# Optimization experiments

Measured on AMD Instinct MI355X. Metric: run time of the kernel, lower is better.

## Reference

```python
import jax, jax.numpy as jnp
import numpy as np

T, B = 21, 4096
H, E, V = 1024, 50, 96
PAD = 0


def setup_inputs() -> dict:
    key = jax.random.key(0)
    ks = jax.random.split(key, 10)
    s_e = 1.0 / np.sqrt(H)  # torch LSTM init scale
    emb = jax.random.normal(ks[0], (V, E), jnp.float32)
    emb = emb.at[PAD].set(0.0)  # padding_idx row is zero
    return {
        "input_ids": jax.random.randint(ks[1], (T, B), 0, V),
        "h0": jax.random.normal(ks[2], (1, B, H), jnp.float32),
        "c0": jax.random.normal(ks[3], (1, B, H), jnp.float32),
        "emb": emb,
        "W_ih": jax.random.uniform(ks[4], (4 * H, E), jnp.float32, -s_e, s_e),
        "W_hh": jax.random.uniform(ks[5], (4 * H, H), jnp.float32, -s_e, s_e),
        "b_ih": jax.random.uniform(ks[6], (4 * H,), jnp.float32, -s_e, s_e),
        "b_hh": jax.random.uniform(ks[7], (4 * H,), jnp.float32, -s_e, s_e),
        "W_out": jax.random.uniform(ks[8], (V, H), jnp.float32, -s_e, s_e),
        "b_out": jax.random.uniform(ks[9], (V,), jnp.float32, -s_e, s_e),
    }


def reference(input_ids, h0, c0, emb, W_ih, W_hh, b_ih, b_hh, W_out, b_out):
    # char_embeds: (T, B, E)
    x = emb[input_ids]
    # Precompute input projections for all timesteps in one GEMM: (T, B, 4H)
    x_proj = jnp.einsum("tbe,ge->tbg", x, W_ih) + b_ih + b_hh

    def step(carry, xp_t):
        h, c = carry  # (B, H) each
        gates = xp_t + h @ W_hh.T  # (B, 4H), torch gate order i,f,g,o
        i, f, g, o = jnp.split(gates, 4, axis=-1)
        i = jax.nn.sigmoid(i)
        f = jax.nn.sigmoid(f)
        g = jnp.tanh(g)
        o = jax.nn.sigmoid(o)
        c = f * c + i * g
        h = o * jnp.tanh(c)
        return (h, c), h

    (h_T, c_T), h_ts = jax.lax.scan(step, (h0[0], c0[0]), x_proj)
    # char_output_projection: (T, B, V)
    scores = jnp.einsum("tbh,vh->tbv", h_ts, W_out) + b_out
    return scores, (h_T[None], c_T[None])
```

## Files before the change

### kernel.cpp

```cpp
#include <hip/hip_runtime.h>
#include <hip/hip_bf16.h>


#define T_STEPS 21
#define BSZ 4096
#define HDIM 1024
#define VOCAB 96
#define EDIM 50

typedef __attribute__((ext_vector_type(8))) short short8;
typedef __attribute__((ext_vector_type(4))) float f32x4;

#define GLL16(g, l)                                                        \
  __builtin_amdgcn_global_load_lds(                                        \
      (const __attribute__((address_space(1))) void*)(g),                  \
      (__attribute__((address_space(3))) void*)(l), 16, 0, 0)

__device__ __forceinline__ float sigmoidf_fast(float x) {
  return 1.0f / (1.0f + __expf(-x));
}
__device__ __forceinline__ float tanhf_fast(float x) {
  return 2.0f / (1.0f + __expf(-2.0f * x)) - 1.0f;
}

__global__ void prep_convert(const float* __restrict__ Whh_f,
                             const float* __restrict__ Wout_f,
                             const float* __restrict__ h0,
                             __hip_bfloat16* __restrict__ Whh,
                             __hip_bfloat16* __restrict__ Wout,
                             __hip_bfloat16* __restrict__ hb0) {
  int idx = blockIdx.x * 256 + threadIdx.x;
  if (idx < 4 * HDIM * HDIM) {
    Whh[idx] = __float2bfloat16(Whh_f[idx]);
    hb0[idx] = __float2bfloat16(h0[idx]);
  }
  if (idx < VOCAB * HDIM) Wout[idx] = __float2bfloat16(Wout_f[idx]);
}

__global__ void prep_ptable(const float* __restrict__ emb,
                            const float* __restrict__ Wih,
                            const float* __restrict__ bih,
                            const float* __restrict__ bhh,
                            __hip_bfloat16* __restrict__ Pb) {
  int idx = blockIdx.x * 256 + threadIdx.x;
  int v = idx >> 12, g = idx & 4095;
  int gate = g >> 10, j = g & 1023;
  const float* er = emb + v * EDIM;
  const float* wr = Wih + g * EDIM;
  float s = bih[g] + bhh[g];
#pragma unroll 10
  for (int e = 0; e < EDIM; ++e) s += er[e] * wr[e];
  Pb[(size_t)(j >> 5) * 12288 + v * 128 + gate * 32 + (j & 31)] =
      __float2bfloat16(s);
}

template <bool LAST>
__global__ __launch_bounds__(256, 3) void lstm_step_kernel(
    const int* __restrict__ ids,
    const __hip_bfloat16* __restrict__ hprev,
    const __hip_bfloat16* __restrict__ Whh,
    const __hip_bfloat16* __restrict__ Pb,
    const float* __restrict__ c_in,
    float* __restrict__ c_out,
    __hip_bfloat16* __restrict__ hnext,
    float* __restrict__ hf32)
{
  __shared__ __align__(16) char smem[32768];
  __hip_bfloat16* sA = (__hip_bfloat16*)smem;
  __hip_bfloat16* sB = (__hip_bfloat16*)(smem + 16384);
  __hip_bfloat16* sPb = (__hip_bfloat16*)smem;

  const int tid = threadIdx.x;
  const int wave = tid >> 6;
  const int lane = tid & 63;
  const int bid = blockIdx.x;
  const int jt = (bid & 7) * 4 + ((bid >> 3) & 3);
  const int mt = bid >> 5;
  const int m0 = mt * 128;
  const int j0 = jt * 32;

  f32x4 acc[4][4] = {};

  const int lrow = lane >> 3;
  const int lcol = ((lane & 7) ^ lrow) * 8;

  int brow_g[4];
#pragma unroll
  for (int i = 0; i < 4; ++i) {
    int n = wave * 32 + i * 8 + lrow;
    int q = n >> 6, gate = (n >> 4) & 3, u = n & 15;
    brow_g[i] = gate * HDIM + j0 + q * 16 + u;
  }
  const __hip_bfloat16* Abase =
      hprev + (size_t)(m0 + wave * 32 + lrow) * HDIM + lcol;

  const int mw = (wave >> 1) * 64;
  const int gn = wave & 1;
  const int u16 = lane & 15;
  const int k16q = lane >> 4;

  const int jo = gn * 16 + u16;
  const int j = j0 + jo;
  const int rb = m0 + mw + k16q * 4;
  float cpre[4][4];
#pragma unroll
  for (int mi = 0; mi < 4; ++mi)
#pragma unroll
    for (int r = 0; r < 4; ++r)
      cpre[mi][r] = c_in[(size_t)(rb + mi * 16 + r) * HDIM + j];

  for (int k0 = 0; k0 < HDIM; k0 += 64) {
#pragma unroll
    for (int i = 0; i < 4; ++i) {
      GLL16(Abase + i * 8 * HDIM + k0, &sA[(wave * 32 + i * 8) * 64]);
      GLL16(Whh + (size_t)brow_g[i] * HDIM + k0 + lcol,
            &sB[(wave * 32 + i * 8) * 64]);
    }
    __syncthreads();
#pragma unroll
    for (int kk = 0; kk < 64; kk += 32) {
      const int sl = (((kk >> 3) + k16q) ^ (u16 & 7)) * 8;
      short8 af[4], bf[4];
#pragma unroll
      for (int mi = 0; mi < 4; ++mi)
        af[mi] = *(const short8*)&sA[(mw + mi * 16 + u16) * 64 + sl];
#pragma unroll
      for (int ni = 0; ni < 4; ++ni)
        bf[ni] = *(const short8*)&sB[(gn * 64 + ni * 16 + u16) * 64 + sl];
#pragma unroll
      for (int mi = 0; mi < 4; ++mi)
#pragma unroll
        for (int ni = 0; ni < 4; ++ni)
          acc[mi][ni] = __builtin_amdgcn_mfma_f32_16x16x32_bf16(
              af[mi], bf[ni], acc[mi][ni], 0, 0, 0);
    }
    __syncthreads();
  }

  {
    const __hip_bfloat16* Pbj = Pb + (size_t)jt * 12288;
#pragma unroll
    for (int i = 0; i < 6; ++i)
      GLL16(Pbj + (wave * 6 + i) * 512 + lane * 8, &sPb[(wave * 6 + i) * 512]);
  }
  __syncthreads();

#pragma unroll
  for (int mi = 0; mi < 4; ++mi) {
#pragma unroll
    for (int r = 0; r < 4; ++r) {
      int row = rb + mi * 16 + r;
      int id = ids[row];
      const __hip_bfloat16* Pr = &sPb[id * 128 + jo];
      float iv = acc[mi][0][r] + __bfloat162float(Pr[0]);
      float fv = acc[mi][1][r] + __bfloat162float(Pr[32]);
      float gv = acc[mi][2][r] + __bfloat162float(Pr[64]);
      float ov = acc[mi][3][r] + __bfloat162float(Pr[96]);
      iv = sigmoidf_fast(iv);
      fv = sigmoidf_fast(fv);
      gv = tanhf_fast(gv);
      ov = sigmoidf_fast(ov);
      size_t off = (size_t)row * HDIM + j;
      float cc = fv * cpre[mi][r] + iv * gv;
      c_out[off] = cc;
      float hh = ov * tanhf_fast(cc);
      hnext[off] = __float2bfloat16(hh);
      if (LAST) hf32[off] = hh;
    }
  }
}

__global__ __launch_bounds__(256, 2) void scores_kernel(
    const __hip_bfloat16* __restrict__ h,
    const __hip_bfloat16* __restrict__ Wout,
    const float* __restrict__ bout,
    float* __restrict__ out)
{
  __shared__ __align__(16) __hip_bfloat16 sA[128 * 128];
  __shared__ __align__(16) __hip_bfloat16 sB[96 * 128];

  const int tid = threadIdx.x;
  const int wave = tid >> 6, lane = tid & 63;
  const int u16 = lane & 15, k16q = lane >> 4;
  const long r0 = (long)blockIdx.x * 128;

  f32x4 acc[2][6] = {};

  const int srow4 = lane >> 4;
  const int sslot = lane & 15;

  for (int k0 = 0; k0 < HDIM; k0 += 128) {
#pragma unroll
    for (int i = 0; i < 8; ++i) {
      int row = wave * 32 + i * 4 + srow4;
      int gg = sslot ^ (row & 15);
      GLL16(h + (r0 + row) * HDIM + k0 + gg * 8, &sA[(wave * 32 + i * 4) * 128]);
    }
#pragma unroll
    for (int i = 0; i < 6; ++i) {
      int row = wave * 24 + i * 4 + srow4;
      int gg = sslot ^ (row & 15);
      GLL16(Wout + (size_t)row * HDIM + k0 + gg * 8,
            &sB[(wave * 24 + i * 4) * 128]);
    }
    __syncthreads();
#pragma unroll
    for (int kk = 0; kk < 128; kk += 32) {
      const int sl = (((kk >> 3) + k16q) ^ u16) * 8;
      short8 af[2], bf[6];
#pragma unroll
      for (int mi = 0; mi < 2; ++mi)
        af[mi] = *(const short8*)&sA[(wave * 32 + mi * 16 + u16) * 128 + sl];
#pragma unroll
      for (int ni = 0; ni < 6; ++ni)
        bf[ni] = *(const short8*)&sB[(ni * 16 + u16) * 128 + sl];
#pragma unroll
      for (int mi = 0; mi < 2; ++mi)
#pragma unroll
        for (int ni = 0; ni < 6; ++ni)
          acc[mi][ni] = __builtin_amdgcn_mfma_f32_16x16x32_bf16(
              af[mi], bf[ni], acc[mi][ni], 0, 0, 0);
    }
    __syncthreads();
  }

#pragma unroll
  for (int ni = 0; ni < 6; ++ni) {
    int v = ni * 16 + u16;
    float bv = bout[v];
#pragma unroll
    for (int mi = 0; mi < 2; ++mi)
#pragma unroll
      for (int r = 0; r < 4; ++r) {
        long grow = r0 + wave * 32 + mi * 16 + k16q * 4 + r;
        out[grow * VOCAB + v] = acc[mi][ni][r] + bv;
      }
  }
}

extern "C" void kernel_launch(void* const* d_in, const int* in_sizes, int n_in,
                              void* d_out, int out_size, void* d_ws, size_t ws_size,
                              hipStream_t stream) {
  const int* ids = (const int*)d_in[0];
  const float* h0 = (const float*)d_in[1];
  const float* c0 = (const float*)d_in[2];
  const float* emb = (const float*)d_in[3];
  const float* Wih = (const float*)d_in[4];
  const float* Whh_f = (const float*)d_in[5];
  const float* bih = (const float*)d_in[6];
  const float* bhh = (const float*)d_in[7];
  const float* Wout_f = (const float*)d_in[8];
  const float* bout = (const float*)d_in[9];

  float* out = (float*)d_out;
  float* scores = out;
  float* hT = out + (size_t)T_STEPS * BSZ * VOCAB;
  float* cT = hT + (size_t)BSZ * HDIM;

  const size_t BH = (size_t)BSZ * HDIM;
  char* w = (char*)d_ws;
  __hip_bfloat16* Pb = (__hip_bfloat16*)w;   w += (size_t)32 * 12288 * 2;
  __hip_bfloat16* Whh = (__hip_bfloat16*)w;  w += (size_t)4 * HDIM * HDIM * 2;
  __hip_bfloat16* Wout = (__hip_bfloat16*)w; w += (size_t)VOCAB * HDIM * 2;
  __hip_bfloat16* hts = (__hip_bfloat16*)w;
  size_t base = (size_t)32 * 12288 * 2 + (size_t)4 * HDIM * HDIM * 2 +
                (size_t)VOCAB * HDIM * 2;
  const bool full = ws_size >= base + (size_t)(T_STEPS + 1) * BH * 2;

  prep_convert<<<dim3((4 * HDIM * HDIM + 255) / 256), dim3(256), 0, stream>>>(
      Whh_f, Wout_f, h0, Whh, Wout, hts);
  prep_ptable<<<dim3((VOCAB * 4096) / 256), dim3(256), 0, stream>>>(
      emb, Wih, bih, bhh, Pb);

  for (int t = 0; t < T_STEPS; ++t) {
    __hip_bfloat16* hp = hts + (full ? (size_t)t * BH : (size_t)(t & 1) * BH);
    __hip_bfloat16* hn =
        hts + (full ? (size_t)(t + 1) * BH : (size_t)((t + 1) & 1) * BH);
    const float* cin = (t == 0) ? c0 : cT;
    if (t == T_STEPS - 1) {
      lstm_step_kernel<true><<<dim3(1024), dim3(256), 0, stream>>>(
          ids + (size_t)t * BSZ, hp, Whh, Pb, cin, cT, hn, hT);
    } else {
      lstm_step_kernel<false><<<dim3(1024), dim3(256), 0, stream>>>(
          ids + (size_t)t * BSZ, hp, Whh, Pb, cin, cT, hn, nullptr);
    }
    if (!full) {
      scores_kernel<<<dim3(BSZ / 128), dim3(256), 0, stream>>>(
          hn, Wout, bout, scores + (size_t)t * BSZ * VOCAB);
    }
  }
  if (full) {
    scores_kernel<<<dim3(T_STEPS * BSZ / 128), dim3(256), 0, stream>>>(
        hts + BH, Wout, bout, scores);
  }
}
```

Before: 1.188 ms.

## Double LSTM step M-tile to 256 rows for W_hh reuse

Each LSTM step block now computes 256 batch rows instead of 128, so every W_hh tile loaded into LDS feeds twice as many MFMAs and the grid halves to 512 blocks. Accumulators, cell-state prefetch and LDS grow to match, and launch bounds drop to 2 blocks per CU. This trades lower weight-load traffic for more register and LDS pressure and fewer blocks to hide latency with (512 blocks against 256 CUs).

```diff
diff --git a/kernel.cpp b/kernel.cpp
--- a/kernel.cpp
+++ b/kernel.cpp
@@ -55,7 +55,7 @@
 }
 
 template <bool LAST>
-__global__ __launch_bounds__(256, 3) void lstm_step_kernel(
+__global__ __launch_bounds__(256, 2) void lstm_step_kernel(
     const int* __restrict__ ids,
     const __hip_bfloat16* __restrict__ hprev,
     const __hip_bfloat16* __restrict__ Whh,
@@ -65,9 +65,9 @@
     __hip_bfloat16* __restrict__ hnext,
     float* __restrict__ hf32)
 {
-  __shared__ __align__(16) char smem[32768];
+  __shared__ __align__(16) char smem[49152];
   __hip_bfloat16* sA = (__hip_bfloat16*)smem;
-  __hip_bfloat16* sB = (__hip_bfloat16*)(smem + 16384);
+  __hip_bfloat16* sB = (__hip_bfloat16*)(smem + 32768);
   __hip_bfloat16* sPb = (__hip_bfloat16*)smem;
 
   const int tid = threadIdx.x;
@@ -76,10 +76,10 @@
   const int bid = blockIdx.x;
   const int jt = (bid & 7) * 4 + ((bid >> 3) & 3);
   const int mt = bid >> 5;
-  const int m0 = mt * 128;
+  const int m0 = mt * 256;
   const int j0 = jt * 32;
 
-  f32x4 acc[4][4] = {};
+  f32x4 acc[2][4][4] = {};
 
   const int lrow = lane >> 3;
   const int lcol = ((lane & 7) ^ lrow) * 8;
@@ -92,7 +92,7 @@
     brow_g[i] = gate * HDIM + j0 + q * 16 + u;
   }
   const __hip_bfloat16* Abase =
-      hprev + (size_t)(m0 + wave * 32 + lrow) * HDIM + lcol;
+      hprev + (size_t)(m0 + wave * 64 + lrow) * HDIM + lcol;
 
   const int mw = (wave >> 1) * 64;
   const int gn = wave & 1;
@@ -101,38 +101,48 @@
 
   const int jo = gn * 16 + u16;
   const int j = j0 + jo;
-  const int rb = m0 + mw + k16q * 4;
-  float cpre[4][4];
-#pragma unroll
-  for (int mi = 0; mi < 4; ++mi)
-#pragma unroll
-    for (int r = 0; r < 4; ++r)
-      cpre[mi][r] = c_in[(size_t)(rb + mi * 16 + r) * HDIM + j];
+  int rb[2];
+  rb[0] = m0 + mw + k16q * 4;
+  rb[1] = m0 + 128 + mw + k16q * 4;
+  float cpre[2][4][4];
+#pragma unroll
+  for (int t = 0; t < 2; ++t)
+#pragma unroll
+    for (int mi = 0; mi < 4; ++mi)
+#pragma unroll
+      for (int r = 0; r < 4; ++r)
+        cpre[t][mi][r] = c_in[(size_t)(rb[t] + mi * 16 + r) * HDIM + j];
 
   for (int k0 = 0; k0 < HDIM; k0 += 64) {
 #pragma unroll
-    for (int i = 0; i < 4; ++i) {
-      GLL16(Abase + i * 8 * HDIM + k0, &sA[(wave * 32 + i * 8) * 64]);
+    for (int i = 0; i < 8; ++i)
+      GLL16(Abase + i * 8 * HDIM + k0, &sA[(wave * 64 + i * 8) * 64]);
+#pragma unroll
+    for (int i = 0; i < 4; ++i)
       GLL16(Whh + (size_t)brow_g[i] * HDIM + k0 + lcol,
             &sB[(wave * 32 + i * 8) * 64]);
-    }
     __syncthreads();
 #pragma unroll
     for (int kk = 0; kk < 64; kk += 32) {
       const int sl = (((kk >> 3) + k16q) ^ (u16 & 7)) * 8;
-      short8 af[4], bf[4];
-#pragma unroll
-      for (int mi = 0; mi < 4; ++mi)
-        af[mi] = *(const short8*)&sA[(mw + mi * 16 + u16) * 64 + sl];
+      short8 af[2][4], bf[4];
+#pragma unroll
+      for (int t = 0; t < 2; ++t)
+#pragma unroll
+        for (int mi = 0; mi < 4; ++mi)
+          af[t][mi] =
+              *(const short8*)&sA[(t * 128 + mw + mi * 16 + u16) * 64 + sl];
 #pragma unroll
       for (int ni = 0; ni < 4; ++ni)
         bf[ni] = *(const short8*)&sB[(gn * 64 + ni * 16 + u16) * 64 + sl];
 #pragma unroll
-      for (int mi = 0; mi < 4; ++mi)
-#pragma unroll
-        for (int ni = 0; ni < 4; ++ni)
-          acc[mi][ni] = __builtin_amdgcn_mfma_f32_16x16x32_bf16(
-              af[mi], bf[ni], acc[mi][ni], 0, 0, 0);
+      for (int t = 0; t < 2; ++t)
+#pragma unroll
+        for (int mi = 0; mi < 4; ++mi)
+#pragma unroll
+          for (int ni = 0; ni < 4; ++ni)
+            acc[t][mi][ni] = __builtin_amdgcn_mfma_f32_16x16x32_bf16(
+                af[t][mi], bf[ni], acc[t][mi][ni], 0, 0, 0);
     }
     __syncthreads();
   }
@@ -146,26 +156,29 @@
   __syncthreads();
 
 #pragma unroll
-  for (int mi = 0; mi < 4; ++mi) {
-#pragma unroll
-    for (int r = 0; r < 4; ++r) {
-      int row = rb + mi * 16 + r;
-      int id = ids[row];
-      const __hip_bfloat16* Pr = &sPb[id * 128 + jo];
-      float iv = acc[mi][0][r] + __bfloat162float(Pr[0]);
-      float fv = acc[mi][1][r] + __bfloat162float(Pr[32]);
-      float gv = acc[mi][2][r] + __bfloat162float(Pr[64]);
-      float ov = acc[mi][3][r] + __bfloat162float(Pr[96]);
-      iv = sigmoidf_fast(iv);
-      fv = sigmoidf_fast(fv);
-      gv = tanhf_fast(gv);
-      ov = sigmoidf_fast(ov);
-      size_t off = (size_t)row * HDIM + j;
-      float cc = fv * cpre[mi][r] + iv * gv;
-      c_out[off] = cc;
-      float hh = ov * tanhf_fast(cc);
-      hnext[off] = __float2bfloat16(hh);
-      if (LAST) hf32[off] = hh;
+  for (int t = 0; t < 2; ++t) {
+#pragma unroll
+    for (int mi = 0; mi < 4; ++mi) {
+#pragma unroll
+      for (int r = 0; r < 4; ++r) {
+        int row = rb[t] + mi * 16 + r;
+        int id = ids[row];
+        const __hip_bfloat16* Pr = &sPb[id * 128 + jo];
+        float iv = acc[t][mi][0][r] + __bfloat162float(Pr[0]);
+        float fv = acc[t][mi][1][r] + __bfloat162float(Pr[32]);
+        float gv = acc[t][mi][2][r] + __bfloat162float(Pr[64]);
+        float ov = acc[t][mi][3][r] + __bfloat162float(Pr[96]);
+        iv = sigmoidf_fast(iv);
+        fv = sigmoidf_fast(fv);
+        gv = tanhf_fast(gv);
+        ov = sigmoidf_fast(ov);
+        size_t off = (size_t)row * HDIM + j;
+        float cc = fv * cpre[t][mi][r] + iv * gv;
+        c_out[off] = cc;
+        float hh = ov * tanhf_fast(cc);
+        hnext[off] = __float2bfloat16(hh);
+        if (LAST) hf32[off] = hh;
+      }
     }
   }
 }
@@ -278,10 +291,10 @@
         hts + (full ? (size_t)(t + 1) * BH : (size_t)((t + 1) & 1) * BH);
     const float* cin = (t == 0) ? c0 : cT;
     if (t == T_STEPS - 1) {
-      lstm_step_kernel<true><<<dim3(1024), dim3(256), 0, stream>>>(
+      lstm_step_kernel<true><<<dim3(512), dim3(256), 0, stream>>>(
           ids + (size_t)t * BSZ, hp, Whh, Pb, cin, cT, hn, hT);
     } else {
-      lstm_step_kernel<false><<<dim3(1024), dim3(256), 0, stream>>>(
+      lstm_step_kernel<false><<<dim3(512), dim3(256), 0, stream>>>(
           ids + (size_t)t * BSZ, hp, Whh, Pb, cin, cT, hn, nullptr);
     }
     if (!full) {
```

New measurement: 1.262 ms. 1.06x slower.

## Replace per-step LSTM launches with one persistent cooperative kernel using grid sync

Applied to the files above, without the earlier changes.

Adds a persistent cooperative kernel of 1056 blocks. 1024 blocks run the recurrent GEMM and gate update for all timesteps, keeping the cell state in registers, and 32 blocks compute the output projection for the previous step at the same time, with grid syncs between steps. This removes the per-step kernel launches and the c-state round trips through global memory, and overlaps the scores GEMM with the recurrence. In exchange it needs all 1056 blocks co-resident (5 per CU at 256 threads) and pays a grid-wide barrier per step. The gate input table is read directly from a float table in global memory instead of being staged in LDS.

```diff
diff --git a/kernel.cpp b/kernel.cpp
--- a/kernel.cpp
+++ b/kernel.cpp
@@ -1,5 +1,8 @@
 #include <hip/hip_runtime.h>
 #include <hip/hip_bf16.h>
+#include <hip/hip_cooperative_groups.h>
+
+namespace cg = cooperative_groups;
 
 
 #define T_STEPS 21
@@ -41,6 +44,7 @@
                             const float* __restrict__ Wih,
                             const float* __restrict__ bih,
                             const float* __restrict__ bhh,
+                            float* __restrict__ P,
                             __hip_bfloat16* __restrict__ Pb) {
   int idx = blockIdx.x * 256 + threadIdx.x;
   int v = idx >> 12, g = idx & 4095;
@@ -50,21 +54,196 @@
   float s = bih[g] + bhh[g];
 #pragma unroll 10
   for (int e = 0; e < EDIM; ++e) s += er[e] * wr[e];
+  P[idx] = s;
   Pb[(size_t)(j >> 5) * 12288 + v * 128 + gate * 32 + (j & 31)] =
       __float2bfloat16(s);
 }
 
+__global__ __launch_bounds__(256, 5) void lstm_persistent(
+    const int* __restrict__ ids_all,
+    const __hip_bfloat16* __restrict__ Whh,
+    const float* __restrict__ P,
+    const __hip_bfloat16* __restrict__ Wout,
+    const float* __restrict__ bout,
+    const float* __restrict__ c0,
+    __hip_bfloat16* __restrict__ h0buf,
+    __hip_bfloat16* __restrict__ h1buf,
+    float* __restrict__ scores,
+    float* __restrict__ hT,
+    float* __restrict__ cT)
+{
+  __shared__ __align__(16) char smem[32768];
+  __hip_bfloat16* sA = (__hip_bfloat16*)smem;
+  __hip_bfloat16* sB = (__hip_bfloat16*)(smem + 16384);
+
+  cg::grid_group gg_grid = cg::this_grid();
+
+  const int tid = threadIdx.x;
+  const int wave = tid >> 6;
+  const int lane = tid & 63;
+  const int bid = blockIdx.x;
+
+  const int lrow = lane >> 3;
+  const int lcol = ((lane & 7) ^ lrow) * 8;
+  const int u16 = lane & 15;
+  const int k16q = lane >> 4;
+
+  if (bid < 1024) {
+    const int jt = (bid & 7) * 4 + ((bid >> 3) & 3);
+    const int mt = bid >> 5;
+    const int m0 = mt * 128;
+    const int j0 = jt * 32;
+    const int mw = (wave >> 1) * 64;
+    const int gn = wave & 1;
+    const int jo = gn * 16 + u16;
+    const int j = j0 + jo;
+    const int rb = m0 + mw + k16q * 4;
+
+    int brow_g[4];
+#pragma unroll
+    for (int i = 0; i < 4; ++i) {
+      int n = wave * 32 + i * 8 + lrow;
+      int q = n >> 6, gate = (n >> 4) & 3, u = n & 15;
+      brow_g[i] = gate * HDIM + j0 + q * 16 + u;
+    }
+
+    float creg[4][4];
+#pragma unroll
+    for (int mi = 0; mi < 4; ++mi)
+#pragma unroll
+      for (int r = 0; r < 4; ++r)
+        creg[mi][r] = c0[(size_t)(rb + mi * 16 + r) * HDIM + j];
+
+    for (int t = 0; t <= T_STEPS; ++t) {
+      if (t < T_STEPS) {
+        const __hip_bfloat16* hprev = (t & 1) ? h1buf : h0buf;
+        __hip_bfloat16* hnext = (t & 1) ? h0buf : h1buf;
+        const int* ids = ids_all + t * BSZ;
+        const __hip_bfloat16* Abase =
+            hprev + (size_t)(m0 + wave * 32 + lrow) * HDIM + lcol;
+
+        f32x4 acc[4][4] = {};
+        for (int k0 = 0; k0 < HDIM; k0 += 64) {
+#pragma unroll
+          for (int i = 0; i < 4; ++i) {
+            GLL16(Abase + i * 8 * HDIM + k0, &sA[(wave * 32 + i * 8) * 64]);
+            GLL16(Whh + (size_t)brow_g[i] * HDIM + k0 + lcol,
+                  &sB[(wave * 32 + i * 8) * 64]);
+          }
+          __syncthreads();
+#pragma unroll
+          for (int kk = 0; kk < 64; kk += 32) {
+            const int sl = (((kk >> 3) + k16q) ^ (u16 & 7)) * 8;
+            short8 af[4], bf[4];
+#pragma unroll
+            for (int mi = 0; mi < 4; ++mi)
+              af[mi] = *(const short8*)&sA[(mw + mi * 16 + u16) * 64 + sl];
+#pragma unroll
+            for (int ni = 0; ni < 4; ++ni)
+              bf[ni] =
+                  *(const short8*)&sB[(gn * 64 + ni * 16 + u16) * 64 + sl];
+#pragma unroll
+            for (int mi = 0; mi < 4; ++mi)
+#pragma unroll
+              for (int ni = 0; ni < 4; ++ni)
+                acc[mi][ni] = __builtin_amdgcn_mfma_f32_16x16x32_bf16(
+                    af[mi], bf[ni], acc[mi][ni], 0, 0, 0);
+          }
+          __syncthreads();
+        }
+
+#pragma unroll
+        for (int mi = 0; mi < 4; ++mi) {
+#pragma unroll
+          for (int r = 0; r < 4; ++r) {
+            int row = rb + mi * 16 + r;
+            int id = ids[row];
+            const float* Pr = P + (size_t)id * 4096 + j;
+            float iv = acc[mi][0][r] + Pr[0];
+            float fv = acc[mi][1][r] + Pr[1024];
+            float gv = acc[mi][2][r] + Pr[2048];
+            float ov = acc[mi][3][r] + Pr[3072];
+            iv = sigmoidf_fast(iv);
+            fv = sigmoidf_fast(fv);
+            gv = tanhf_fast(gv);
+            ov = sigmoidf_fast(ov);
+            float cc = fv * creg[mi][r] + iv * gv;
+            creg[mi][r] = cc;
+            float hh = ov * tanhf_fast(cc);
+            size_t off = (size_t)row * HDIM + j;
+            hnext[off] = __float2bfloat16(hh);
+            if (t == T_STEPS - 1) {
+              hT[off] = hh;
+              cT[off] = cc;
+            }
+          }
+        }
+      }
+      if (t < T_STEPS) gg_grid.sync();
+    }
+  } else {
+    const int sb = bid - 1024;
+    const long r0 = (long)sb * 128;
+    for (int t = 0; t <= T_STEPS; ++t) {
+      if (t >= 1) {
+        const __hip_bfloat16* h = (t & 1) ? h1buf : h0buf;
+        float* out = scores + (size_t)(t - 1) * BSZ * VOCAB;
+        f32x4 acc[2][6] = {};
+        for (int k0 = 0; k0 < HDIM; k0 += 64) {
+#pragma unroll
+          for (int i = 0; i < 4; ++i)
+            GLL16(h + (r0 + wave * 32 + i * 8 + lrow) * HDIM + k0 + lcol,
+                  &sA[(wave * 32 + i * 8) * 64]);
+#pragma unroll
+          for (int i = 0; i < 3; ++i)
+            GLL16(Wout + (size_t)(wave * 24 + i * 8 + lrow) * HDIM + k0 + lcol,
+                  &sB[(wave * 24 + i * 8) * 64]);
+          __syncthreads();
+#pragma unroll
+          for (int kk = 0; kk < 64; kk += 32) {
+            const int sl = (((kk >> 3) + k16q) ^ (u16 & 7)) * 8;
+            short8 af[2], bf[6];
+#pragma unroll
+            for (int mi = 0; mi < 2; ++mi)
+              af[mi] =
+                  *(const short8*)&sA[(wave * 32 + mi * 16 + u16) * 64 + sl];
+#pragma unroll
+            for (int ni = 0; ni < 6; ++ni)
+              bf[ni] = *(const short8*)&sB[(ni * 16 + u16) * 64 + sl];
+#pragma unroll
+            for (int mi = 0; mi < 2; ++mi)
+#pragma unroll
+              for (int ni = 0; ni < 6; ++ni)
+                acc[mi][ni] = __builtin_amdgcn_mfma_f32_16x16x32_bf16(
+                    af[mi], bf[ni], acc[mi][ni], 0, 0, 0);
+          }
+          __syncthreads();
+        }
+#pragma unroll
+        for (int ni = 0; ni < 6; ++ni) {
+          int v = ni * 16 + u16;
+          float bv = bout[v];
+#pragma unroll
+          for (int mi = 0; mi < 2; ++mi)
+#pragma unroll
+            for (int r = 0; r < 4; ++r) {
+              long grow = r0 + wave * 32 + mi * 16 + k16q * 4 + r;
+              out[grow * VOCAB + v] = acc[mi][ni][r] + bv;
+            }
+        }
+      }
+      if (t < T_STEPS) gg_grid.sync();
+    }
+  }
+}
+
 template <bool LAST>
 __global__ __launch_bounds__(256, 3) void lstm_step_kernel(
-    const int* __restrict__ ids,
-    const __hip_bfloat16* __restrict__ hprev,
+    const int* __restrict__ ids, const __hip_bfloat16* __restrict__ hprev,
     const __hip_bfloat16* __restrict__ Whh,
-    const __hip_bfloat16* __restrict__ Pb,
-    const float* __restrict__ c_in,
-    float* __restrict__ c_out,
-    __hip_bfloat16* __restrict__ hnext,
-    float* __restrict__ hf32)
-{
+    const __hip_bfloat16* __restrict__ Pb, const float* __restrict__ c_in,
+    float* __restrict__ c_out, __hip_bfloat16* __restrict__ hnext,
+    float* __restrict__ hf32) {
   __shared__ __align__(16) char smem[32768];
   __hip_bfloat16* sA = (__hip_bfloat16*)smem;
   __hip_bfloat16* sB = (__hip_bfloat16*)(smem + 16384);
@@ -80,7 +259,6 @@
   const int j0 = jt * 32;
 
   f32x4 acc[4][4] = {};
-
   const int lrow = lane >> 3;
   const int lcol = ((lane & 7) ^ lrow) * 8;
 
@@ -98,7 +276,6 @@
   const int gn = wave & 1;
   const int u16 = lane & 15;
   const int k16q = lane >> 4;
-
   const int jo = gn * 16 + u16;
   const int j = j0 + jo;
   const int rb = m0 + mw + k16q * 4;
@@ -136,7 +313,6 @@
     }
     __syncthreads();
   }
-
   {
     const __hip_bfloat16* Pbj = Pb + (size_t)jt * 12288;
 #pragma unroll
@@ -144,7 +320,6 @@
       GLL16(Pbj + (wave * 6 + i) * 512 + lane * 8, &sPb[(wave * 6 + i) * 512]);
   }
   __syncthreads();
-
 #pragma unroll
   for (int mi = 0; mi < 4; ++mi) {
 #pragma unroll
@@ -171,36 +346,30 @@
 }
 
 __global__ __launch_bounds__(256, 2) void scores_kernel(
-    const __hip_bfloat16* __restrict__ h,
-    const __hip_bfloat16* __restrict__ Wout,
-    const float* __restrict__ bout,
-    float* __restrict__ out)
-{
+    const __hip_bfloat16* __restrict__ h, const __hip_bfloat16* __restrict__ Wout,
+    const float* __restrict__ bout, float* __restrict__ out) {
   __shared__ __align__(16) __hip_bfloat16 sA[128 * 128];
   __shared__ __align__(16) __hip_bfloat16 sB[96 * 128];
-
   const int tid = threadIdx.x;
   const int wave = tid >> 6, lane = tid & 63;
   const int u16 = lane & 15, k16q = lane >> 4;
   const long r0 = (long)blockIdx.x * 128;
-
   f32x4 acc[2][6] = {};
-
   const int srow4 = lane >> 4;
   const int sslot = lane & 15;
-
   for (int k0 = 0; k0 < HDIM; k0 += 128) {
 #pragma unroll
     for (int i = 0; i < 8; ++i) {
       int row = wave * 32 + i * 4 + srow4;
-      int gg = sslot ^ (row & 15);
-      GLL16(h + (r0 + row) * HDIM + k0 + gg * 8, &sA[(wave * 32 + i * 4) * 128]);
+      int gg2 = sslot ^ (row & 15);
+      GLL16(h + (r0 + row) * HDIM + k0 + gg2 * 8,
+            &sA[(wave * 32 + i * 4) * 128]);
     }
 #pragma unroll
     for (int i = 0; i < 6; ++i) {
       int row = wave * 24 + i * 4 + srow4;
-      int gg = sslot ^ (row & 15);
-      GLL16(Wout + (size_t)row * HDIM + k0 + gg * 8,
+      int gg2 = sslot ^ (row & 15);
+      GLL16(Wout + (size_t)row * HDIM + k0 + gg2 * 8,
             &sB[(wave * 24 + i * 4) * 128]);
     }
     __syncthreads();
@@ -223,7 +392,6 @@
     }
     __syncthreads();
   }
-
 #pragma unroll
   for (int ni = 0; ni < 6; ++ni) {
     int v = ni * 16 + u16;
@@ -259,38 +427,52 @@
 
   const size_t BH = (size_t)BSZ * HDIM;
   char* w = (char*)d_ws;
+  float* P = (float*)w;                      w += (size_t)VOCAB * 4096 * 4;
   __hip_bfloat16* Pb = (__hip_bfloat16*)w;   w += (size_t)32 * 12288 * 2;
   __hip_bfloat16* Whh = (__hip_bfloat16*)w;  w += (size_t)4 * HDIM * HDIM * 2;
   __hip_bfloat16* Wout = (__hip_bfloat16*)w; w += (size_t)VOCAB * HDIM * 2;
-  __hip_bfloat16* hts = (__hip_bfloat16*)w;
-  size_t base = (size_t)32 * 12288 * 2 + (size_t)4 * HDIM * HDIM * 2 +
-                (size_t)VOCAB * HDIM * 2;
-  const bool full = ws_size >= base + (size_t)(T_STEPS + 1) * BH * 2;
+  __hip_bfloat16* h0b = (__hip_bfloat16*)w;  w += BH * 2;
+  __hip_bfloat16* h1b = (__hip_bfloat16*)w;  w += BH * 2;
 
   prep_convert<<<dim3((4 * HDIM * HDIM + 255) / 256), dim3(256), 0, stream>>>(
-      Whh_f, Wout_f, h0, Whh, Wout, hts);
+      Whh_f, Wout_f, h0, Whh, Wout, h0b);
   prep_ptable<<<dim3((VOCAB * 4096) / 256), dim3(256), 0, stream>>>(
-      emb, Wih, bih, bhh, Pb);
-
-  for (int t = 0; t < T_STEPS; ++t) {
-    __hip_bfloat16* hp = hts + (full ? (size_t)t * BH : (size_t)(t & 1) * BH);
-    __hip_bfloat16* hn =
-        hts + (full ? (size_t)(t + 1) * BH : (size_t)((t + 1) & 1) * BH);
-    const float* cin = (t == 0) ? c0 : cT;
-    if (t == T_STEPS - 1) {
-      lstm_step_kernel<true><<<dim3(1024), dim3(256), 0, stream>>>(
-          ids + (size_t)t * BSZ, hp, Whh, Pb, cin, cT, hn, hT);
-    } else {
-      lstm_step_kernel<false><<<dim3(1024), dim3(256), 0, stream>>>(
-          ids + (size_t)t * BSZ, hp, Whh, Pb, cin, cT, hn, nullptr);
-    }
-    if (!full) {
+      emb, Wih, bih, bhh, P, Pb);
+
+  int per_cu = 0;
+  hipError_t oe = hipOccupancyMaxActiveBlocksPerMultiprocessor(
+      &per_cu, (const void*)lstm_persistent, 256, 0);
+  bool coop = (oe == hipSuccess) && ((long)per_cu * 256 >= 1056);
+
+  if (coop) {
+    const int* a0 = ids;
+    const __hip_bfloat16* a1 = Whh;
+    const float* a2 = P;
+    const __hip_bfloat16* a3 = Wout;
+    const float* a4 = bout;
+    const float* a5 = c0;
+    __hip_bfloat16* a6 = h0b;
+    __hip_bfloat16* a7 = h1b;
+    float* a8 = scores;
+    float* a9 = hT;
+    float* a10 = cT;
+    void* args[] = {&a0, &a1, &a2, &a3, &a4, &a5, &a6, &a7, &a8, &a9, &a10};
+    hipLaunchCooperativeKernel((void*)lstm_persistent, dim3(1056), dim3(256),
+                               args, 0, stream);
+  } else {
+    for (int t = 0; t < T_STEPS; ++t) {
+      __hip_bfloat16* hp = (t & 1) ? h1b : h0b;
+      __hip_bfloat16* hn = (t & 1) ? h0b : h1b;
+      const float* cin = (t == 0) ? c0 : cT;
+      if (t == T_STEPS - 1) {
+        lstm_step_kernel<true><<<dim3(1024), dim3(256), 0, stream>>>(
+            ids + (size_t)t * BSZ, hp, Whh, Pb, cin, cT, hn, hT);
+      } else {
+        lstm_step_kernel<false><<<dim3(1024), dim3(256), 0, stream>>>(
+            ids + (size_t)t * BSZ, hp, Whh, Pb, cin, cT, hn, nullptr);
+      }
       scores_kernel<<<dim3(BSZ / 128), dim3(256), 0, stream>>>(
           hn, Wout, bout, scores + (size_t)t * BSZ * VOCAB);
     }
   }
-  if (full) {
-    scores_kernel<<<dim3(T_STEPS * BSZ / 128), dim3(256), 0, stream>>>(
-        hts + BH, Wout, bout, scores);
-  }
-}
+}
```

New measurement: 1.391 ms. 17.1% more time.

## Double-buffer LDS tiles in LSTM step GEMM with async prefetch

Applied to the files above, without the earlier changes.

Converts the K-loop of the per-timestep recurrent GEMM into a double-buffered pipeline. The next 64-wide tile of h and W_hh is loaded into the alternate LDS buffer while MFMAs run on the current one, with explicit vmcnt waits and raw s_barrier in place of __syncthreads. This is meant to hide global-to-LDS load latency. In exchange, LDS use doubles to 64KB and launch bounds drop from 3 to 2 blocks per CU, which lowers occupancy.

```diff
diff --git a/kernel.cpp b/kernel.cpp
--- a/kernel.cpp
+++ b/kernel.cpp
@@ -15,6 +15,10 @@
   __builtin_amdgcn_global_load_lds(                                        \
       (const __attribute__((address_space(1))) void*)(g),                  \
       (__attribute__((address_space(3))) void*)(l), 16, 0, 0)
+
+#define ASM_BARRIER() asm volatile("s_barrier" ::: "memory")
+#define ASM_VMCNT8() asm volatile("s_waitcnt vmcnt(8)" ::: "memory")
+#define ASM_VMCNT0() asm volatile("s_waitcnt vmcnt(0)" ::: "memory")
 
 __device__ __forceinline__ float sigmoidf_fast(float x) {
   return 1.0f / (1.0f + __expf(-x));
@@ -55,7 +59,7 @@
 }
 
 template <bool LAST>
-__global__ __launch_bounds__(256, 3) void lstm_step_kernel(
+__global__ __launch_bounds__(256, 2) void lstm_step_kernel(
     const int* __restrict__ ids,
     const __hip_bfloat16* __restrict__ hprev,
     const __hip_bfloat16* __restrict__ Whh,
@@ -65,9 +69,7 @@
     __hip_bfloat16* __restrict__ hnext,
     float* __restrict__ hf32)
 {
-  __shared__ __align__(16) char smem[32768];
-  __hip_bfloat16* sA = (__hip_bfloat16*)smem;
-  __hip_bfloat16* sB = (__hip_bfloat16*)(smem + 16384);
+  __shared__ __align__(16) char smem[65536];
   __hip_bfloat16* sPb = (__hip_bfloat16*)smem;
 
   const int tid = threadIdx.x;
@@ -93,6 +95,7 @@
   }
   const __hip_bfloat16* Abase =
       hprev + (size_t)(m0 + wave * 32 + lrow) * HDIM + lcol;
+  const __hip_bfloat16* Bbase = Whh + lcol;
 
   const int mw = (wave >> 1) * 64;
   const int gn = wave & 1;
@@ -109,24 +112,51 @@
     for (int r = 0; r < 4; ++r)
       cpre[mi][r] = c_in[(size_t)(rb + mi * 16 + r) * HDIM + j];
 
-  for (int k0 = 0; k0 < HDIM; k0 += 64) {
+  const int sSlotA = wave * 32 * 64;
+  const int sSlotB = wave * 32 * 64;
+
+  {
+    __hip_bfloat16* nA = (__hip_bfloat16*)smem;
+    __hip_bfloat16* nB = (__hip_bfloat16*)(smem + 16384);
 #pragma unroll
     for (int i = 0; i < 4; ++i) {
-      GLL16(Abase + i * 8 * HDIM + k0, &sA[(wave * 32 + i * 8) * 64]);
-      GLL16(Whh + (size_t)brow_g[i] * HDIM + k0 + lcol,
-            &sB[(wave * 32 + i * 8) * 64]);
-    }
-    __syncthreads();
+      GLL16(Abase + i * 8 * HDIM, &nA[sSlotA + i * 8 * 64]);
+      GLL16(Bbase + (size_t)brow_g[i] * HDIM, &nB[sSlotB + i * 8 * 64]);
+    }
+  }
+
+  for (int it = 0; it < 16; ++it) {
+    char* curb = smem + ((it & 1) << 15);
+    char* nxtb = smem + ((~it & 1) << 15);
+    const __hip_bfloat16* cA = (const __hip_bfloat16*)curb;
+    const __hip_bfloat16* cB = (const __hip_bfloat16*)(curb + 16384);
+
+    ASM_BARRIER();
+    if (it < 15) {
+      __hip_bfloat16* nA = (__hip_bfloat16*)nxtb;
+      __hip_bfloat16* nB = (__hip_bfloat16*)(nxtb + 16384);
+      const int k0 = (it + 1) * 64;
+#pragma unroll
+      for (int i = 0; i < 4; ++i) {
+        GLL16(Abase + i * 8 * HDIM + k0, &nA[sSlotA + i * 8 * 64]);
+        GLL16(Bbase + (size_t)brow_g[i] * HDIM + k0, &nB[sSlotB + i * 8 * 64]);
+      }
+      ASM_VMCNT8();
+    } else {
+      ASM_VMCNT0();
+    }
+    ASM_BARRIER();
+
 #pragma unroll
     for (int kk = 0; kk < 64; kk += 32) {
       const int sl = (((kk >> 3) + k16q) ^ (u16 & 7)) * 8;
       short8 af[4], bf[4];
 #pragma unroll
       for (int mi = 0; mi < 4; ++mi)
-        af[mi] = *(const short8*)&sA[(mw + mi * 16 + u16) * 64 + sl];
+        af[mi] = *(const short8*)&cA[(mw + mi * 16 + u16) * 64 + sl];
 #pragma unroll
       for (int ni = 0; ni < 4; ++ni)
-        bf[ni] = *(const short8*)&sB[(gn * 64 + ni * 16 + u16) * 64 + sl];
+        bf[ni] = *(const short8*)&cB[(gn * 64 + ni * 16 + u16) * 64 + sl];
 #pragma unroll
       for (int mi = 0; mi < 4; ++mi)
 #pragma unroll
@@ -134,7 +164,6 @@
           acc[mi][ni] = __builtin_amdgcn_mfma_f32_16x16x32_bf16(
               af[mi], bf[ni], acc[mi][ni], 0, 0, 0);
     }
-    __syncthreads();
   }
 
   {
```

New measurement: 1.114 ms. -6.2%, faster.
